# Kernel optimization log

Hardware: AMD Instinct MI355X
Metric: run time of the kernel (lower is better)

Reference implementation:

```python
import jax, jax.numpy as jnp
import numpy as np
from jax import lax

K = 8          # num_classes
C_IN = 256     # in_channels
EPS = 1e-5


def resize_bilinear_ac(x, H, W):
    """Bilinear resize with align_corners=True. x: [B,C,h,w] -> [B,C,H,W]."""
    B, C, h, w = x.shape
    if h == H and w == W:
        return x
    ys = jnp.linspace(0.0, h - 1.0, H)
    xs = jnp.linspace(0.0, w - 1.0, W)
    y0 = jnp.floor(ys).astype(jnp.int32)
    x0 = jnp.floor(xs).astype(jnp.int32)
    y1 = jnp.minimum(y0 + 1, h - 1)
    x1 = jnp.minimum(x0 + 1, w - 1)
    wy = (ys - y0.astype(x.dtype))[None, None, :, None]
    wx = (xs - x0.astype(x.dtype))[None, None, None, :]
    g00 = x[:, :, y0][:, :, :, x0]
    g01 = x[:, :, y0][:, :, :, x1]
    g10 = x[:, :, y1][:, :, :, x0]
    g11 = x[:, :, y1][:, :, :, x1]
    top = g00 * (1.0 - wx) + g01 * wx
    bot = g10 * (1.0 - wx) + g11 * wx
    return top * (1.0 - wy) + bot * wy


def setup_inputs() -> dict:
    key = jax.random.key(0)
    ks = jax.random.split(key, 16)
    shapes = [(2, 256, 128, 128), (2, 256, 64, 64), (2, 256, 32, 32), (2, 256, 16, 16), (2, 256, 8, 8)]
    inp = {}
    for i, s in enumerate(shapes):
        inp[f"feat{i}"] = jax.random.normal(ks[i], s, dtype=jnp.float32)
    inp["attr_feat"] = jax.random.normal(ks[5], (2, K * C_IN, 64, 64), dtype=jnp.float32)
    # learned params
    inp["mlp_f_w"] = jax.random.normal(ks[6], (256, 256), dtype=jnp.float32) * 0.02
    inp["mlp_f_b"] = jnp.zeros((256,), dtype=jnp.float32)
    inp["mlp_a_w"] = jax.random.normal(ks[7], (256, 256), dtype=jnp.float32) * 0.02
    inp["mlp_a_b"] = jnp.zeros((256,), dtype=jnp.float32)
    # 5 grouped convs: [out=2048, in_per_group=256, 3, 3] each, no bias (BN follows)
    inp["conv_w"] = jax.random.normal(ks[8], (5, K * C_IN, C_IN, 3, 3), dtype=jnp.float32) * 0.02
    inp["bn_gamma"] = jnp.ones((5, K * C_IN), dtype=jnp.float32)
    inp["bn_beta"] = jnp.zeros((5, K * C_IN), dtype=jnp.float32)
    inp["bn_mean"] = jax.random.normal(ks[9], (5, K * C_IN), dtype=jnp.float32) * 0.1
    inp["bn_var"] = jax.random.uniform(ks[10], (5, K * C_IN), dtype=jnp.float32, minval=0.5, maxval=1.5)
    return inp


def _forward(feats, attr_feat, mlp_f_w, mlp_f_b, mlp_a_w, mlp_a_b, conv_w, bn_gamma, bn_beta, bn_mean, bn_var):
    B = attr_feat.shape[0]
    # global avg pool attr -> [B, K, C] -> mlp_a
    avg_attr = attr_feat.mean(axis=(2, 3)).reshape(B, K, C_IN)
    avg_attr = avg_attr @ mlp_a_w.T + mlp_a_b  # [B,K,256]
    outs = []
    for i, x in enumerate(feats):
        _, C, H, W = x.shape
        avg_x = x.mean(axis=(2, 3)) @ mlp_f_w.T + mlp_f_b          # [B,256]
        logits = jnp.einsum('bkc,bc->bk', avg_attr, avg_x)          # [B,K]
        attn = jax.nn.softmax(logits, axis=-1)
        y = resize_bilinear_ac(attr_feat, H, W)                      # [B,2048,H,W]
        y = lax.conv_general_dilated(
            y, conv_w[i], window_strides=(1, 1), padding=((1, 1), (1, 1)),
            dimension_numbers=('NCHW', 'OIHW', 'NCHW'), feature_group_count=K)
        inv = lax.rsqrt(bn_var[i] + EPS)
        y = (y - bn_mean[i][None, :, None, None]) * (inv * bn_gamma[i])[None, :, None, None] + bn_beta[i][None, :, None, None]
        y = jax.nn.relu(y)
        y = y.reshape(B, K, C, H, W)
        y = jnp.einsum('bkchw,bk->bchw', y, attn)                   # weighted sum over classes
        outs.append(jax.nn.relu(x + y))
    return tuple(outs)


def reference(feat0, feat1, feat2, feat3, feat4, attr_feat, mlp_f_w, mlp_f_b, mlp_a_w, mlp_a_b, conv_w, bn_gamma, bn_beta, bn_mean, bn_var):
    feats = [feat0, feat1, feat2, feat3, feat4]
    return _forward(feats, attr_feat, mlp_f_w, mlp_f_b, mlp_a_w, mlp_a_b, conv_w, bn_gamma, bn_beta, bn_mean, bn_var)
```

## Files before the change

### kernel.cpp

```cpp
#include <hip/hip_runtime.h>
#include <hip/hip_bf16.h>
#include <cstdint>

typedef __attribute__((ext_vector_type(8))) short short8;
typedef __attribute__((ext_vector_type(4))) float f32x4;

#define EPSV 1e-5f

__device__ __forceinline__ void gload_lds16(const void* g, void* l) {
  __builtin_amdgcn_global_load_lds(
      (const __attribute__((address_space(1))) void*)(uintptr_t)g,
      (__attribute__((address_space(3))) void*)(uint32_t)(uintptr_t)l,
      16, 0, 0);
}

__global__ void mean_kernel(const float* __restrict__ in, float* __restrict__ out,
                            int HW, float inv) {
  const int ch = blockIdx.x;
  const int t = threadIdx.x;
  const float* p = in + (size_t)ch * HW;
  float s = 0.f;
  const int nv = HW >> 2;
  const float4* pv = (const float4*)p;
  for (int i = t; i < nv; i += 256) { float4 v = pv[i]; s += v.x + v.y + v.z + v.w; }
  __shared__ float red[256];
  red[t] = s; __syncthreads();
  for (int off = 128; off > 0; off >>= 1) {
    if (t < off) red[t] += red[t + off];
    __syncthreads();
  }
  if (t == 0) out[ch] = red[0] * inv;
}

__global__ void wtrans_kernel(const float* __restrict__ cw,
                              const float* __restrict__ gamma, const float* __restrict__ beta,
                              const float* __restrict__ mean, const float* __restrict__ var,
                              __hip_bfloat16* __restrict__ wt, float* __restrict__ bias) {
  const int oc = blockIdx.x;
  const int i  = blockIdx.y;
  const int ci = threadIdx.x;
  const int idx = i * 2048 + oc;
  const float sc = rsqrtf(var[idx] + EPSV) * gamma[idx];
  if (ci == 0) bias[idx] = beta[idx] - mean[idx] * sc;
  const int g = oc >> 8, co = oc & 255;
  const float* src = cw + ((size_t)idx * 256 + ci) * 9;
  const size_t dbase = (size_t)(i * 8 + g) * 9 * 65536 + co * 256 + ci;
#pragma unroll
  for (int tap = 0; tap < 9; ++tap)
    wt[dbase + (size_t)tap * 65536] = __float2bfloat16(src[tap] * sc);
}

__global__ void gate_kernel(const float* __restrict__ meanA, const float* __restrict__ meanF,
                            const float* __restrict__ Wa, const float* __restrict__ ba,
                            const float* __restrict__ Wf, const float* __restrict__ bfp,
                            float* __restrict__ attn) {
  __shared__ float mA[16 * 256];
  __shared__ float mF[10 * 256];
  __shared__ float pA[16 * 256];
  __shared__ float pF[10 * 256];
  __shared__ float lg[80];
  const int t = threadIdx.x;
  for (int i = t; i < 4096; i += 256) mA[i] = meanA[i];
  for (int i = t; i < 2560; i += 256) mF[i] = meanF[i];
  __syncthreads();
  {
    float acc[16];
#pragma unroll
    for (int j = 0; j < 16; ++j) acc[j] = 0.f;
    for (int ci = 0; ci < 256; ++ci) {
      const float w = Wa[t * 256 + ci];
#pragma unroll
      for (int j = 0; j < 16; ++j) acc[j] += mA[j * 256 + ci] * w;
    }
    const float bb = ba[t];
#pragma unroll
    for (int j = 0; j < 16; ++j) pA[j * 256 + t] = acc[j] + bb;
  }
  {
    float acc[10];
#pragma unroll
    for (int j = 0; j < 10; ++j) acc[j] = 0.f;
    for (int ci = 0; ci < 256; ++ci) {
      const float w = Wf[t * 256 + ci];
#pragma unroll
      for (int j = 0; j < 10; ++j) acc[j] += mF[j * 256 + ci] * w;
    }
    const float bb = bfp[t];
#pragma unroll
    for (int j = 0; j < 10; ++j) pF[j * 256 + t] = acc[j] + bb;
  }
  __syncthreads();
  if (t < 80) {
    const int i = t >> 4, r = t & 15, b = r >> 3, k = r & 7;
    const float* a = &pA[(b * 8 + k) * 256];
    const float* f = &pF[(i * 2 + b) * 256];
    float d = 0.f;
    for (int c = 0; c < 256; ++c) d += a[c] * f[c];
    lg[t] = d;
  }
  __syncthreads();
  if (t < 10) {
    const int base = t * 8;
    float m = lg[base];
    for (int k = 1; k < 8; ++k) m = fmaxf(m, lg[base + k]);
    float e[8], s = 0.f;
    for (int k = 0; k < 8; ++k) { e[k] = __expf(lg[base + k] - m); s += e[k]; }
    const float invs = 1.f / s;
    for (int k = 0; k < 8; ++k) attn[base + k] = e[k] * invs;
  }
}

__global__ void resize_kernel(const float* __restrict__ attr,
                              __hip_bfloat16* __restrict__ R,
                              int W, int Hp, int Wp, float scl) {
  const int bk = blockIdx.x;
  const int yp = blockIdx.y;
  const int t  = threadIdx.x;
  const size_t rowbase = ((size_t)bk * Hp + yp) * (size_t)Wp * 256;
  if (yp == 0 || yp == Hp - 1) {
    uint32_t* p = (uint32_t*)(R + rowbase);
    const int n = Wp * 128;
    for (int idx = t; idx < n; idx += 256) p[idx] = 0u;
    return;
  }
  const int y = yp - 1;
  const float fy = y * scl;
  int y0 = (int)floorf(fy); if (y0 > 63) y0 = 63;
  const float wy = fy - (float)y0;
  const int y1 = min(y0 + 1, 63);
  __shared__ float buf[2][64][65];
  const int cc = t >> 2, seg = (t & 3) * 16;
  const int bb = bk >> 3, k = bk & 7;
  const float* ab = attr + (size_t)bb * 2048 * 4096;
  const int ci = t & 63;
  for (int cq = 0; cq < 4; ++cq) {
    __syncthreads();
    {
      const int ch = k * 256 + cq * 64 + cc;
      const float* r0 = ab + ((size_t)ch * 64 + y0) * 64;
      const float* r1 = ab + ((size_t)ch * 64 + y1) * 64;
#pragma unroll
      for (int u = 0; u < 4; ++u) {
        float4 v0 = ((const float4*)r0)[(t & 3) * 4 + u];
        float4 v1 = ((const float4*)r1)[(t & 3) * 4 + u];
        buf[0][cc][seg + u * 4 + 0] = v0.x; buf[0][cc][seg + u * 4 + 1] = v0.y;
        buf[0][cc][seg + u * 4 + 2] = v0.z; buf[0][cc][seg + u * 4 + 3] = v0.w;
        buf[1][cc][seg + u * 4 + 0] = v1.x; buf[1][cc][seg + u * 4 + 1] = v1.y;
        buf[1][cc][seg + u * 4 + 2] = v1.z; buf[1][cc][seg + u * 4 + 3] = v1.w;
      }
    }
    __syncthreads();
    for (int x = t >> 6; x < W; x += 4) {
      const float fx = x * scl;
      int x0 = (int)floorf(fx); if (x0 > 63) x0 = 63;
      const float wx = fx - (float)x0;
      const int x1 = min(x0 + 1, 63);
      const float top = buf[0][ci][x0] * (1.f - wx) + buf[0][ci][x1] * wx;
      const float bot = buf[1][ci][x0] * (1.f - wx) + buf[1][ci][x1] * wx;
      R[rowbase + (size_t)(x + 1) * 256 + cq * 64 + ci] = __float2bfloat16(top * (1.f - wy) + bot * wy);
    }
    if (t < 64) {
      R[rowbase + cq * 64 + t] = __float2bfloat16(0.f);
      R[rowbase + (size_t)(Wp - 1) * 256 + cq * 64 + t] = __float2bfloat16(0.f);
    }
  }
}

__global__ __launch_bounds__(256, 2)
void conv_kernel(const __hip_bfloat16* __restrict__ R,
                 const __hip_bfloat16* __restrict__ Wt,
                 const float* __restrict__ bias,
                 const float* __restrict__ attn,
                 const float* __restrict__ featp,
                 float* __restrict__ outp,
                 int W, int lw, int Hp, int Wp, int HW,
                 int b0, int NB, int gcount) {
  __shared__ alignas(16) __hip_bfloat16 ldsA[128 * 64];
  __shared__ alignas(16) __hip_bfloat16 ldsB[128 * 64];
  const int tid  = threadIdx.x;
  const int lane = tid & 63;
  const int wave = __builtin_amdgcn_readfirstlane(tid >> 6);
  const int wm = (wave >> 1) * 64;
  const int wn = (wave & 1) * 64;
  const int co0 = blockIdx.y * 128;
  const int n0  = blockIdx.x * 128;
  const int bb  = (int)blockIdx.z % NB;
  const int gs  = (int)blockIdx.z / NB;
  const int b   = b0 + bb;
  const int g0  = gs * gcount;

  const int c8 = lane & 7;
  const int r8 = lane >> 3;
  int aoff[4], boff[4];
#pragma unroll
  for (int q = 0; q < 4; ++q) {
    const int row = (wave * 4 + q) * 8 + r8;
    const int sc = (c8 ^ (row & 7)) << 3;
    aoff[q] = ((co0 + row) << 8) + sc;
    int sg = n0 + row; if (sg >= HW) sg = HW - 1;
    const int y = sg >> lw, x = sg & (W - 1);
    boff[q] = (y * Wp + x) * 256 + sc;
  }

  const f32x4 fz = {0.f, 0.f, 0.f, 0.f};
  f32x4 fin[4][4];
#pragma unroll
  for (int mf = 0; mf < 4; ++mf)
#pragma unroll
    for (int nf = 0; nf < 4; ++nf) fin[mf][nf] = fz;

  for (int g = g0; g < g0 + gcount; ++g) {
    f32x4 acc[4][4];
#pragma unroll
    for (int mf = 0; mf < 4; ++mf)
#pragma unroll
      for (int nf = 0; nf < 4; ++nf) acc[mf][nf] = fz;

    const __hip_bfloat16* Wg = Wt + (size_t)g * 9 * 65536;
    const __hip_bfloat16* Rg = R + (size_t)(bb * 8 + g) * Hp * Wp * 256;

    for (int ty = 0; ty < 3; ++ty)
      for (int tx = 0; tx < 3; ++tx) {
        const __hip_bfloat16* Wtap = Wg + (size_t)(ty * 3 + tx) * 65536;
        const __hip_bfloat16* Rtap = Rg + (ty * Wp + tx) * 256;
        for (int cq = 0; cq < 4; ++cq) {
          const int cqo = cq * 64;
          __syncthreads();
#pragma unroll
          for (int q = 0; q < 4; ++q) {
            gload_lds16(Wtap + aoff[q] + cqo, &ldsA[(wave * 4 + q) * 512]);
            gload_lds16(Rtap + boff[q] + cqo, &ldsB[(wave * 4 + q) * 512]);
          }
          __syncthreads();
#pragma unroll
          for (int ks = 0; ks < 2; ++ks) {
            short8 af[4], bfv[4];
            const int cb = ks * 4 + (lane >> 4);
#pragma unroll
            for (int mf = 0; mf < 4; ++mf) {
              const int row = wm + mf * 16 + (lane & 15);
              af[mf] = *(const short8*)&ldsA[(row << 6) + ((cb ^ (row & 7)) << 3)];
            }
#pragma unroll
            for (int nf = 0; nf < 4; ++nf) {
              const int row = wn + nf * 16 + (lane & 15);
              bfv[nf] = *(const short8*)&ldsB[(row << 6) + ((cb ^ (row & 7)) << 3)];
            }
#pragma unroll
            for (int mf = 0; mf < 4; ++mf)
#pragma unroll
              for (int nf = 0; nf < 4; ++nf)
                acc[mf][nf] = __builtin_amdgcn_mfma_f32_16x16x32_bf16(
                    af[mf], bfv[nf], acc[mf][nf], 0, 0, 0);
          }
        }
      }

    const float aw = attn[b * 8 + g];
#pragma unroll
    for (int mf = 0; mf < 4; ++mf) {
      const int cobase = co0 + wm + mf * 16 + ((lane >> 4) << 2);
#pragma unroll
      for (int r = 0; r < 4; ++r) {
        const float bs = bias[(g << 8) + cobase + r];
#pragma unroll
        for (int nf = 0; nf < 4; ++nf)
          fin[mf][nf][r] += aw * fmaxf(acc[mf][nf][r] + bs, 0.f);
      }
    }
  }

  const size_t plane = (size_t)256 * HW;
  if (featp) {
    const float* fb = featp + (size_t)b * plane;
    float* ob = outp + (size_t)b * plane;
#pragma unroll
    for (int mf = 0; mf < 4; ++mf) {
      const int cobase = co0 + wm + mf * 16 + ((lane >> 4) << 2);
#pragma unroll
      for (int nf = 0; nf < 4; ++nf) {
        const int n = n0 + wn + nf * 16 + (lane & 15);
        if (n < HW) {
#pragma unroll
          for (int r = 0; r < 4; ++r) {
            const size_t idx = (size_t)(cobase + r) * HW + n;
            ob[idx] = fmaxf(fb[idx] + fin[mf][nf][r], 0.f);
          }
        }
      }
    }
  } else {
    float* zb = outp + ((size_t)gs * 2 + b) * plane;
#pragma unroll
    for (int mf = 0; mf < 4; ++mf) {
      const int cobase = co0 + wm + mf * 16 + ((lane >> 4) << 2);
#pragma unroll
      for (int nf = 0; nf < 4; ++nf) {
        const int n = n0 + wn + nf * 16 + (lane & 15);
        if (n < HW) {
#pragma unroll
          for (int r = 0; r < 4; ++r)
            zb[(size_t)(cobase + r) * HW + n] = fin[mf][nf][r];
        }
      }
    }
  }
}

__global__ void reduce_kernel(const float* __restrict__ z, const float* __restrict__ feat,
                              float* __restrict__ outp, int total, int S) {
  const int idx = blockIdx.x * 256 + threadIdx.x;
  if (idx >= total) return;
  float s = feat[idx];
  for (int j = 0; j < S; ++j) s += z[(size_t)j * total + idx];
  outp[idx] = fmaxf(s, 0.f);
}

extern "C" void kernel_launch(void* const* d_in, const int* in_sizes, int n_in,
                              void* d_out, int out_size, void* d_ws, size_t ws_size,
                              hipStream_t stream) {
  const float* feat[5];
  for (int i = 0; i < 5; ++i) feat[i] = (const float*)d_in[i];
  const float* attr = (const float*)d_in[5];
  const float* mfw = (const float*)d_in[6];
  const float* mfb = (const float*)d_in[7];
  const float* maw = (const float*)d_in[8];
  const float* mab = (const float*)d_in[9];
  const float* cw  = (const float*)d_in[10];
  const float* bng = (const float*)d_in[11];
  const float* bnb = (const float*)d_in[12];
  const float* bnm = (const float*)d_in[13];
  const float* bnv = (const float*)d_in[14];
  float* out = (float*)d_out;

  char* ws = (char*)d_ws;
  float* attnW = (float*)(ws);
  float* meanA = (float*)(ws + 512);
  float* meanF = (float*)(ws + 20480);
  float* biasW = (float*)(ws + 32768);
  __hip_bfloat16* Wt = (__hip_bfloat16*)(ws + 131072);
  const size_t R_OFF = 47316992;
  __hip_bfloat16* Rbuf = (__hip_bfloat16*)(ws + R_OFF);

  const bool full = ws_size >= (size_t)219316224;
  const int NB = full ? 2 : 1;
  float* zbuf = (float*)(ws + R_OFF + (size_t)NB * 69222400);

  static const int HS[5] = {128, 64, 32, 16, 8};
  static const size_t OOFF[5] = {0, 8388608, 10485760, 11010048, 11141120};
  static const int SPLIT[5] = {1, 4, 8, 8, 8};

  mean_kernel<<<4096, 256, 0, stream>>>(attr, meanA, 4096, 1.f / 4096.f);
  for (int i = 0; i < 5; ++i) {
    const int HW = HS[i] * HS[i];
    mean_kernel<<<512, 256, 0, stream>>>(feat[i], meanF + i * 512, HW, 1.f / (float)HW);
  }
  wtrans_kernel<<<dim3(2048, 5), 256, 0, stream>>>(cw, bng, bnb, bnm, bnv, Wt, biasW);
  gate_kernel<<<1, 256, 0, stream>>>(meanA, meanF, maw, mab, mfw, mfb, attnW);

  for (int i = 0; i < 5; ++i) {
    const int H = HS[i], W = H, HW = H * W, Hp = H + 2, Wp = W + 2;
    const int lw = 31 - __builtin_clz((unsigned)W);
    const float scl = 63.f / (float)(H - 1);
    const int S = full ? SPLIT[i] : 1;
    const int gcount = 8 / S;
    for (int b0 = 0; b0 < 2; b0 += NB) {
      resize_kernel<<<dim3(NB * 8, Hp), 256, 0, stream>>>(
          attr + (size_t)b0 * 2048 * 4096, Rbuf, W, Hp, Wp, scl);
      const float* fp = (S == 1) ? feat[i] : nullptr;
      float* op = (S == 1) ? (out + OOFF[i]) : zbuf;
      conv_kernel<<<dim3((HW + 127) / 128, 2, NB * S), 256, 0, stream>>>(
          Rbuf, Wt + (size_t)i * 8 * 9 * 65536, biasW + i * 2048, attnW + i * 16,
          fp, op, W, lw, Hp, Wp, HW, b0, NB, gcount);
    }
    if (S > 1) {
      const int total = 2 * 256 * HW;
      reduce_kernel<<<(total + 255) / 256, 256, 0, stream>>>(zbuf, feat[i], out + OOFF[i], total, S);
    }
  }
}
```

Measured before the change: 850.0 us.

## Double-buffer LDS tiles in conv kernel to overlap global loads with MFMA

```diff
diff --git a/kernel.cpp b/kernel.cpp
--- a/kernel.cpp
+++ b/kernel.cpp
@@ -175,8 +175,8 @@
                  float* __restrict__ outp,
                  int W, int lw, int Hp, int Wp, int HW,
                  int b0, int NB, int gcount) {
-  __shared__ alignas(16) __hip_bfloat16 ldsA[128 * 64];
-  __shared__ alignas(16) __hip_bfloat16 ldsB[128 * 64];
+  __shared__ alignas(16) __hip_bfloat16 ldsA[2][128 * 64];
+  __shared__ alignas(16) __hip_bfloat16 ldsB[2][128 * 64];
   const int tid  = threadIdx.x;
   const int lane = tid & 63;
   const int wave = __builtin_amdgcn_readfirstlane(tid >> 6);
@@ -202,71 +202,93 @@
     boff[q] = (y * Wp + x) * 256 + sc;
   }
 
+  const size_t rgstride = (size_t)Hp * Wp * 256;
+  const __hip_bfloat16* Rb = R + (size_t)bb * 8 * rgstride;
+
   const f32x4 fz = {0.f, 0.f, 0.f, 0.f};
-  f32x4 fin[4][4];
+  f32x4 fin[4][4], acc[4][4];
 #pragma unroll
   for (int mf = 0; mf < 4; ++mf)
 #pragma unroll
-    for (int nf = 0; nf < 4; ++nf) fin[mf][nf] = fz;
-
-  for (int g = g0; g < g0 + gcount; ++g) {
-    f32x4 acc[4][4];
-#pragma unroll
-    for (int mf = 0; mf < 4; ++mf)
-#pragma unroll
-      for (int nf = 0; nf < 4; ++nf) acc[mf][nf] = fz;
-
-    const __hip_bfloat16* Wg = Wt + (size_t)g * 9 * 65536;
-    const __hip_bfloat16* Rg = R + (size_t)(bb * 8 + g) * Hp * Wp * 256;
-
-    for (int ty = 0; ty < 3; ++ty)
-      for (int tx = 0; tx < 3; ++tx) {
-        const __hip_bfloat16* Wtap = Wg + (size_t)(ty * 3 + tx) * 65536;
-        const __hip_bfloat16* Rtap = Rg + (ty * Wp + tx) * 256;
-        for (int cq = 0; cq < 4; ++cq) {
-          const int cqo = cq * 64;
-          __syncthreads();
-#pragma unroll
-          for (int q = 0; q < 4; ++q) {
-            gload_lds16(Wtap + aoff[q] + cqo, &ldsA[(wave * 4 + q) * 512]);
-            gload_lds16(Rtap + boff[q] + cqo, &ldsB[(wave * 4 + q) * 512]);
-          }
-          __syncthreads();
-#pragma unroll
-          for (int ks = 0; ks < 2; ++ks) {
-            short8 af[4], bfv[4];
-            const int cb = ks * 4 + (lane >> 4);
-#pragma unroll
-            for (int mf = 0; mf < 4; ++mf) {
-              const int row = wm + mf * 16 + (lane & 15);
-              af[mf] = *(const short8*)&ldsA[(row << 6) + ((cb ^ (row & 7)) << 3)];
-            }
-#pragma unroll
-            for (int nf = 0; nf < 4; ++nf) {
-              const int row = wn + nf * 16 + (lane & 15);
-              bfv[nf] = *(const short8*)&ldsB[(row << 6) + ((cb ^ (row & 7)) << 3)];
-            }
-#pragma unroll
-            for (int mf = 0; mf < 4; ++mf)
-#pragma unroll
-              for (int nf = 0; nf < 4; ++nf)
-                acc[mf][nf] = __builtin_amdgcn_mfma_f32_16x16x32_bf16(
-                    af[mf], bfv[nf], acc[mf][nf], 0, 0, 0);
+    for (int nf = 0; nf < 4; ++nf) { fin[mf][nf] = fz; acc[mf][nf] = fz; }
+
+  {
+    const __hip_bfloat16* wp = Wt + ((size_t)g0 * 9 << 16);
+    const __hip_bfloat16* rp = Rb + (size_t)g0 * rgstride;
+#pragma unroll
+    for (int q = 0; q < 4; ++q) {
+      gload_lds16(wp + aoff[q], &ldsA[0][(wave * 4 + q) * 512]);
+      gload_lds16(rp + boff[q], &ldsB[0][(wave * 4 + q) * 512]);
+    }
+  }
+  int cqp = 0, txp = 0, typ = 0, gp = g0;
+  int foldc = 0, gcur = g0;
+  const int nstages = gcount * 36;
+
+  for (int s = 0; s < nstages; ++s) {
+    __builtin_amdgcn_s_barrier();
+    asm volatile("" ::: "memory");
+    if (s + 1 < nstages) {
+      ++cqp;
+      if (cqp == 4) {
+        cqp = 0; ++txp;
+        if (txp == 3) { txp = 0; ++typ; if (typ == 3) { typ = 0; ++gp; } }
+      }
+      const __hip_bfloat16* wp = Wt + (((size_t)gp * 9 + typ * 3 + txp) << 16) + (cqp << 6);
+      const __hip_bfloat16* rp = Rb + (size_t)gp * rgstride + ((typ * Wp + txp) << 8) + (cqp << 6);
+      const int nb = (s + 1) & 1;
+#pragma unroll
+      for (int q = 0; q < 4; ++q) {
+        gload_lds16(wp + aoff[q], &ldsA[nb][(wave * 4 + q) * 512]);
+        gload_lds16(rp + boff[q], &ldsB[nb][(wave * 4 + q) * 512]);
+      }
+      asm volatile("s_waitcnt vmcnt(8)" ::: "memory");
+    } else {
+      asm volatile("s_waitcnt vmcnt(0)" ::: "memory");
+    }
+    __builtin_amdgcn_s_barrier();
+    asm volatile("" ::: "memory");
+
+    const int cb0 = s & 1;
+#pragma unroll
+    for (int ks = 0; ks < 2; ++ks) {
+      short8 af[4], bfv[4];
+      const int cb = ks * 4 + (lane >> 4);
+#pragma unroll
+      for (int mf = 0; mf < 4; ++mf) {
+        const int row = wm + mf * 16 + (lane & 15);
+        af[mf] = *(const short8*)&ldsA[cb0][(row << 6) + ((cb ^ (row & 7)) << 3)];
+      }
+#pragma unroll
+      for (int nf = 0; nf < 4; ++nf) {
+        const int row = wn + nf * 16 + (lane & 15);
+        bfv[nf] = *(const short8*)&ldsB[cb0][(row << 6) + ((cb ^ (row & 7)) << 3)];
+      }
+#pragma unroll
+      for (int mf = 0; mf < 4; ++mf)
+#pragma unroll
+        for (int nf = 0; nf < 4; ++nf)
+          acc[mf][nf] = __builtin_amdgcn_mfma_f32_16x16x32_bf16(
+              af[mf], bfv[nf], acc[mf][nf], 0, 0, 0);
+    }
+
+    if (++foldc == 36) {
+      foldc = 0;
+      const float aw = attn[b * 8 + gcur];
+#pragma unroll
+      for (int mf = 0; mf < 4; ++mf) {
+        const int cobase = co0 + wm + mf * 16 + ((lane >> 4) << 2);
+#pragma unroll
+        for (int r = 0; r < 4; ++r) {
+          const float bs = bias[(gcur << 8) + cobase + r];
+#pragma unroll
+          for (int nf = 0; nf < 4; ++nf) {
+            fin[mf][nf][r] += aw * fmaxf(acc[mf][nf][r] + bs, 0.f);
+            acc[mf][nf][r] = 0.f;
           }
         }
       }
-
-    const float aw = attn[b * 8 + g];
-#pragma unroll
-    for (int mf = 0; mf < 4; ++mf) {
-      const int cobase = co0 + wm + mf * 16 + ((lane >> 4) << 2);
-#pragma unroll
-      for (int r = 0; r < 4; ++r) {
-        const float bs = bias[(g << 8) + cobase + r];
-#pragma unroll
-        for (int nf = 0; nf < 4; ++nf)
-          fin[mf][nf][r] += aw * fmaxf(acc[mf][nf][r] + bs, 0.f);
-      }
+      ++gcur;
     }
   }
 
```

Result: faster. 751.0 us (-11.6%).
